# Kernel tuning notes

Hardware: AMD Instinct MI355X
Metric: run time of the kernel (lower is better)

## Reference

```python
import jax, jax.numpy as jnp
import numpy as np


def _ring_mask(n, d, dtype):
    # concentric-square mask: ring index r = min(i, j, n-1-i, n-1-j);
    # outer d rings are 0, inner rings are 1; center forced to 1.
    i = jnp.arange(n)
    ri = jnp.minimum(i, n - 1 - i)  # [n]
    ring = jnp.minimum(ri[:, None], ri[None, :])  # [n, n]
    mask = (ring >= d).astype(dtype)
    w = (n + 1) // 2
    mask = mask.at[w - 1, w - 1].set(jnp.asarray(1, dtype))
    return mask


def _conv2d(x, w, b):
    # x: [B,1,2,C], w: [1,1,2,k] -> [B,1,1,C] (padding only along last axis)
    pad = (w.shape[3] - 1) // 2
    y = jax.lax.conv_general_dilated(
        x, w, window_strides=(1, 1), padding=((0, 0), (pad, pad)),
        dimension_numbers=('NCHW', 'OIHW', 'NCHW'))
    return y + b.reshape(1, 1, 1, 1)


def setup_inputs() -> dict:
    key = jax.random.key(0)
    k1, k2, k3, k4, k5 = jax.random.split(key, 5)
    B, C1, C2, P = 512, 16, 30, 15
    K = 5  # int((log2(480)+3)/2) made odd
    x = jax.random.normal(k1, (B, C1, C2, P, P), dtype=jnp.float32)
    w1 = jax.random.normal(k2, (1, 1, 2, K), dtype=jnp.float32) * 0.3
    b1 = jax.random.normal(k3, (1,), dtype=jnp.float32) * 0.1
    w2 = jax.random.normal(k4, (1, 1, 2, K), dtype=jnp.float32) * 0.3
    b2 = jax.random.normal(k5, (1,), dtype=jnp.float32) * 0.1
    return {"x": x, "w1": w1, "b1": b1, "w2": w2, "b2": b2}


def reference(x, w1, b1, w2, b2):
    B, C1, C2, H, W = x.shape
    C = C1 * C2
    out = x.reshape(B, C, H, W)
    d = (W - 1) // 2 - 1  # patch_size == W, ScaleMaskModule d
    mask = _ring_mask(W, d, x.dtype)  # [W, W]

    # masked branch: adaptive avg pool(1) == spatial mean of masked input
    out_x1 = (out * mask).mean(axis=(2, 3))  # [B, C]
    out_x2 = out_x1[:, ::-1]                 # reversed channel order
    out_xx = jnp.stack([out_x1, out_x2], axis=1)[:, None]  # [B,1,2,C]

    # plain branch
    out1 = out.mean(axis=(2, 3))  # [B, C]
    out2 = out1[:, ::-1]
    outx = jnp.stack([out1, out2], axis=1)[:, None]  # [B,1,2,C]

    a1 = jax.nn.sigmoid(_conv2d(outx, w1, b1))    # [B,1,1,C]
    a2 = jax.nn.sigmoid(_conv2d(out_xx, w2, b2))  # [B,1,1,C]
    at1 = jnp.transpose(a1 * a2, (0, 3, 1, 2))    # [B,C,1,1]
    at = jax.nn.sigmoid((at1 - 0.2) * 2)

    out = out * at
    return out.reshape(B, C1, C2, H, W)
```

## Files before the change

kernel.cpp:

```cpp
#include <hip/hip_runtime.h>
#include <math.h>

#define BB 512
#define CC 480
#define HW 225
#define CHW (CC * HW)
#define NF4 (CHW / 4)
#define NGRP (CC / 4)
#define NGRP_TOTAL (BB * NGRP)

#define RED_BLOCKS 1920
#define RED_THREADS 256
#define RED_WAVES (RED_BLOCKS * (RED_THREADS / 64))

#define CHUNKS 8
#define CHUNK_F4 (NF4 / CHUNKS)
#define CHUNK_CH (CC / CHUNKS)
#define SC_THREADS 256
#define SC_FULL_ITERS (CHUNK_F4 / SC_THREADS)
#define SC_TAIL (CHUNK_F4 - SC_FULL_ITERS * SC_THREADS)

using f4 = __attribute__((ext_vector_type(4))) float;

__device__ __forceinline__ float sigmoidf(float v) {
    return 1.0f / (1.0f + __expf(-v));
}

__global__ __launch_bounds__(RED_THREADS) void reduce_kernel(
    const float* __restrict__ x,
    float* __restrict__ S)
{
    const int wave = threadIdx.x >> 6;
    const int lane = threadIdx.x & 63;
    const int gw0 = blockIdx.x * (RED_THREADS / 64) + wave;

    for (int gg = gw0; gg < NGRP_TOTAL; gg += RED_WAVES) {
        const int b  = gg / NGRP;
        const int gr = gg - b * NGRP;
        const f4* __restrict__ gp = (const f4*)x + (long long)b * NF4 + gr * 225;

        float f0 = 0.f, f1 = 0.f, f2 = 0.f, f3 = 0.f;
#pragma unroll
        for (int j = 0; j < 4; ++j) {
            const int idx = lane + 64 * j;
            if (idx < 225) {
                f4 v = gp[idx];
                const float s1 = v[0] + v[1];
                const float s2 = s1 + v[2];
                const float hs = s2 + v[3];
                const int q = (idx >= 113) ? ((idx >= 169) ? 3 : 2)
                                           : ((idx >= 57) ? 1 : 0);
                const float lo = (idx == 56) ? v[0]
                               : (idx == 112) ? s1
                               : (idx == 168) ? s2 : hs;
                const float hi = hs - lo;
                f0 += (q == 0) ? lo : 0.f;
                f1 += (q == 1) ? lo : 0.f;
                f2 += (q == 2) ? lo : 0.f;
                f3 += (q == 3) ? lo : 0.f;
                f1 += (q == 0) ? hi : 0.f;
                f2 += (q == 1) ? hi : 0.f;
                f3 += (q == 2) ? hi : 0.f;
            }
        }
#pragma unroll
        for (int off = 32; off > 0; off >>= 1) {
            f0 += __shfl_down(f0, off, 64);
            f1 += __shfl_down(f1, off, 64);
            f2 += __shfl_down(f2, off, 64);
            f3 += __shfl_down(f3, off, 64);
        }
        if (lane == 0) {
            const float s = 1.0f / 225.0f;
            const int base = b * CC + 4 * gr;
            S[base + 0] = f0 * s;
            S[base + 1] = f1 * s;
            S[base + 2] = f2 * s;
            S[base + 3] = f3 * s;
        }
    }
}

__global__ __launch_bounds__(512) void gate_kernel(
    const float* __restrict__ x,
    const float* __restrict__ S,
    const float* __restrict__ w1, const float* __restrict__ b1,
    const float* __restrict__ w2, const float* __restrict__ b2,
    float* __restrict__ G)
{
    __shared__ float Rs[CC];
    const int b = blockIdx.x;
    const int c = threadIdx.x;

    if (c < CC) {
        const float* __restrict__ ch = x + (long long)b * CHW + c * HW;
        const float r = ((ch[96] + ch[97] + ch[98])
                       + (ch[111] + ch[112] + ch[113]))
                       + (ch[126] + ch[127] + ch[128]);
        Rs[c] = r * (1.0f / 225.0f);
    }
    __syncthreads();

    if (c < CC) {
        const float* __restrict__ Ms = S + b * CC;
        float g1 = b1[0], g2 = b2[0];
#pragma unroll
        for (int k = 0; k < 5; ++k) {
            const int j = c + k - 2;
            if (j >= 0 && j < CC) {
                g1 += w1[k] * Ms[j] + w1[5 + k] * Ms[CC - 1 - j];
                g2 += w2[k] * Rs[j] + w2[5 + k] * Rs[CC - 1 - j];
            }
        }
        G[b * CC + c] = sigmoidf((sigmoidf(g1) * sigmoidf(g2) - 0.2f) * 2.0f);
    }
}

__global__ __launch_bounds__(SC_THREADS) void scale_kernel(
    const float* __restrict__ x, const float* __restrict__ G,
    float* __restrict__ out)
{
    __shared__ float As[CHUNK_CH];
    const int blk = blockIdx.x;
    const int b = blk >> 3;
    const int s = blk & 7;
    const int t = threadIdx.x;

    if (t < CHUNK_CH) As[t] = G[b * CC + s * CHUNK_CH + t];
    __syncthreads();

    const f4* __restrict__ xb = (const f4*)x + (long long)b * NF4 + s * CHUNK_F4;
    f4* __restrict__ ob = (f4*)out + (long long)b * NF4 + s * CHUNK_F4;

#pragma unroll 4
    for (int k = 0; k < SC_FULL_ITERS; ++k) {
        const int g = t + SC_THREADS * k;
        f4 v = xb[g];
        const int e = 4 * g;
        const int c = e / 225;
        const int rr = e - 225 * c;
        v[0] *= As[c];
        v[1] *= As[c + (rr >= 224)];
        v[2] *= As[c + (rr >= 223)];
        v[3] *= As[c + (rr >= 222)];
        __builtin_nontemporal_store(v, &ob[g]);
    }
    if (t < SC_TAIL) {
        const int g = SC_FULL_ITERS * SC_THREADS + t;
        f4 v = xb[g];
        const int e = 4 * g;
        const int c = e / 225;
        const int rr = e - 225 * c;
        v[0] *= As[c];
        v[1] *= As[c + (rr >= 224)];
        v[2] *= As[c + (rr >= 223)];
        v[3] *= As[c + (rr >= 222)];
        __builtin_nontemporal_store(v, &ob[g]);
    }
}

extern "C" void kernel_launch(void* const* d_in, const int* in_sizes, int n_in,
                              void* d_out, int out_size, void* d_ws, size_t ws_size,
                              hipStream_t stream)
{
    const float* x  = (const float*)d_in[0];
    const float* w1 = (const float*)d_in[1];
    const float* b1 = (const float*)d_in[2];
    const float* w2 = (const float*)d_in[3];
    const float* b2 = (const float*)d_in[4];
    float* out = (float*)d_out;

    float* S = (float*)d_ws;
    float* G = S + BB * CC;

    reduce_kernel<<<RED_BLOCKS, RED_THREADS, 0, stream>>>(x, S);
    gate_kernel<<<BB, 512, 0, stream>>>(x, S, w1, b1, w2, b2, G);
    scale_kernel<<<BB * CHUNKS, SC_THREADS, 0, stream>>>(x, G, out);
}
```

Baseline: 416.0 us.

## Fuse gate computation into scale kernel and use regular stores

Merges the gate kernel into the scale kernel. Each 60-channel chunk block now computes its own gate values from the reduced means and the 3x3 center sums it reads for its channel window plus halo and the mirrored channels. This drops one kernel launch and the global round trip through the gate buffer. Output stores also switch from nontemporal to regular stores. The cost is some redundant center-value reads in each block and an extra barrier before the scaling loop.

```diff
diff --git a/kernel.cpp b/kernel.cpp
--- a/kernel.cpp
+++ b/kernel.cpp
@@ -81,27 +81,37 @@
     }
 }
 
-__global__ __launch_bounds__(512) void gate_kernel(
-    const float* __restrict__ x,
-    const float* __restrict__ S,
+__global__ __launch_bounds__(SC_THREADS) void scalegate_kernel(
+    const float* __restrict__ x, const float* __restrict__ S,
     const float* __restrict__ w1, const float* __restrict__ b1,
     const float* __restrict__ w2, const float* __restrict__ b2,
-    float* __restrict__ G)
+    float* __restrict__ out)
 {
-    __shared__ float Rs[CC];
-    const int b = blockIdx.x;
-    const int c = threadIdx.x;
+    __shared__ float RW[64];
+    __shared__ float RM[64];
+    __shared__ float As[CHUNK_CH];
 
-    if (c < CC) {
-        const float* __restrict__ ch = x + (long long)b * CHW + c * HW;
-        const float r = ((ch[96] + ch[97] + ch[98])
-                       + (ch[111] + ch[112] + ch[113]))
-                       + (ch[126] + ch[127] + ch[128]);
-        Rs[c] = r * (1.0f / 225.0f);
+    const int blk = blockIdx.x;
+    const int b = blk >> 3;
+    const int s = blk & 7;
+    const int C0 = s * CHUNK_CH;
+    const int t = threadIdx.x;
+
+    if (t < 128) {
+        const int ch = (t < 64) ? (C0 - 2 + t) : (418 - C0 + (t - 64));
+        float rm = 0.f;
+        if ((unsigned)ch < (unsigned)CC) {
+            const float* __restrict__ chp = x + (long long)b * CHW + ch * HW;
+            rm = (((chp[96] + chp[97] + chp[98])
+                 + (chp[111] + chp[112] + chp[113]))
+                 + (chp[126] + chp[127] + chp[128])) * (1.0f / 225.0f);
+        }
+        if (t < 64) RW[t] = rm; else RM[t - 64] = rm;
     }
     __syncthreads();
 
-    if (c < CC) {
+    if (t < CHUNK_CH) {
+        const int c = C0 + t;
         const float* __restrict__ Ms = S + b * CC;
         float g1 = b1[0], g2 = b2[0];
 #pragma unroll
@@ -109,24 +119,11 @@
             const int j = c + k - 2;
             if (j >= 0 && j < CC) {
                 g1 += w1[k] * Ms[j] + w1[5 + k] * Ms[CC - 1 - j];
-                g2 += w2[k] * Rs[j] + w2[5 + k] * Rs[CC - 1 - j];
+                g2 += w2[k] * RW[j - (C0 - 2)] + w2[5 + k] * RM[C0 + 61 - j];
             }
         }
-        G[b * CC + c] = sigmoidf((sigmoidf(g1) * sigmoidf(g2) - 0.2f) * 2.0f);
+        As[t] = sigmoidf((sigmoidf(g1) * sigmoidf(g2) - 0.2f) * 2.0f);
     }
-}
-
-__global__ __launch_bounds__(SC_THREADS) void scale_kernel(
-    const float* __restrict__ x, const float* __restrict__ G,
-    float* __restrict__ out)
-{
-    __shared__ float As[CHUNK_CH];
-    const int blk = blockIdx.x;
-    const int b = blk >> 3;
-    const int s = blk & 7;
-    const int t = threadIdx.x;
-
-    if (t < CHUNK_CH) As[t] = G[b * CC + s * CHUNK_CH + t];
     __syncthreads();
 
     const f4* __restrict__ xb = (const f4*)x + (long long)b * NF4 + s * CHUNK_F4;
@@ -143,7 +140,7 @@
         v[1] *= As[c + (rr >= 224)];
         v[2] *= As[c + (rr >= 223)];
         v[3] *= As[c + (rr >= 222)];
-        __builtin_nontemporal_store(v, &ob[g]);
+        ob[g] = v;
     }
     if (t < SC_TAIL) {
         const int g = SC_FULL_ITERS * SC_THREADS + t;
@@ -155,7 +152,7 @@
         v[1] *= As[c + (rr >= 224)];
         v[2] *= As[c + (rr >= 223)];
         v[3] *= As[c + (rr >= 222)];
-        __builtin_nontemporal_store(v, &ob[g]);
+        ob[g] = v;
     }
 }
 
@@ -171,9 +168,8 @@
     float* out = (float*)d_out;
 
     float* S = (float*)d_ws;
-    float* G = S + BB * CC;
 
     reduce_kernel<<<RED_BLOCKS, RED_THREADS, 0, stream>>>(x, S);
-    gate_kernel<<<BB, 512, 0, stream>>>(x, S, w1, b1, w2, b2, G);
-    scale_kernel<<<BB * CHUNKS, SC_THREADS, 0, stream>>>(x, G, out);
+    scalegate_kernel<<<BB * CHUNKS, SC_THREADS, 0, stream>>>(
+        x, S, w1, b1, w2, b2, out);
 }
```

New measurement: 436.3 us. +4.9%, slower.
